# Performance work log

Hardware: AMD Instinct MI355X
Metric: run time of the kernel (lower is better)

The kernel has to match this reference:

```python
import jax, jax.numpy as jnp
import numpy as np

B, T, C, H = 4, 4096, 384, 64

def setup_inputs() -> dict:
    key = jax.random.key(0)
    ks = jax.random.split(key, 7)
    return {
        "x": jax.random.normal(ks[0], (B, T, C), dtype=jnp.float32),
        "Wk": jax.random.normal(ks[1], (H, C), dtype=jnp.float32) * 0.05,
        "bk": jax.random.normal(ks[2], (H,), dtype=jnp.float32) * 0.05,
        "Wq": jax.random.normal(ks[3], (H, C), dtype=jnp.float32) * 0.05,
        "bq": jax.random.normal(ks[4], (H,), dtype=jnp.float32) * 0.05,
        "Wv": jax.random.normal(ks[5], (H, C), dtype=jnp.float32) * 0.05,
        "bv": jax.random.normal(ks[6], (H,), dtype=jnp.float32) * 0.05,
    }

def reference(x, Wk, bk, Wq, bq, Wv, bv):
    # Faithful to the source, including its quirks:
    #   - q = self.value(x)   (query uses the VALUE projection; Wq/bq unused)
    #   - scale = C ** -0.5 with C = embedding dim (384), not head dim
    #   - dropout in eval mode (identity)
    Bb, Tt, Cc = x.shape
    k = x @ Wk.T + bk                                  # (B,T,H)
    q = x @ Wv.T + bv                                  # (B,T,H)  <- bug reproduced
    scale = jnp.float32(Cc) ** -0.5
    scores = jnp.einsum('bth,bsh->bts', q, k) * scale  # (B,T,T)
    mask = jnp.tril(jnp.ones((Tt, Tt), dtype=bool))    # causal mask
    scores = jnp.where(mask, scores, jnp.float32(-jnp.inf))
    w = jax.nn.softmax(scores, axis=-1)                # (B,T,T)
    v = x @ Wv.T + bv                                  # (B,T,H)
    return jnp.einsum('bts,bsh->bth', w, v)            # (B,T,H)
```

## Files before the change

### kernel.cpp

```cpp
#include <hip/hip_runtime.h>

#define T_SEQ 4096
#define CDIM 384

typedef __attribute__((ext_vector_type(8))) short short8;
typedef __attribute__((ext_vector_type(4))) short short4e;
typedef __attribute__((ext_vector_type(4))) float float4e;

#define KSCALE 0.05103103630798288f
#define KE (KSCALE * 1.4426950408889634f)

__device__ inline unsigned short f2bf(float f) {
  unsigned u = __builtin_bit_cast(unsigned, f);
  u += 0x7FFFu + ((u >> 16) & 1u);
  return (unsigned short)(u >> 16);
}

__device__ inline void dma16(const void* g, void* l) {
  __builtin_amdgcn_global_load_lds(
      (const __attribute__((address_space(1))) unsigned int*)g,
      (__attribute__((address_space(3))) unsigned int*)l, 16, 0, 0);
}

__global__ __launch_bounds__(128) void proj_kernel(
    const float* __restrict__ x, const float* __restrict__ Wk, const float* __restrict__ bk,
    const float* __restrict__ Wv, const float* __restrict__ bv,
    unsigned short* __restrict__ Ktil, unsigned short* __restrict__ Qrow,
    unsigned short* __restrict__ Vtil) {
  __shared__ alignas(16) unsigned short Wl[2][128 * 40];
  const int tid = threadIdx.x;
  const int lane = tid & 63;
  const int w = tid >> 6;
  const int lid = lane & 15, quad = lane >> 4;
  const int rowbase = blockIdx.x * 32 + w * 16;
  const float* xr = x + (size_t)(rowbase + lid) * CDIM;

  float4e wreg[8];
  int wcol[8], wpart[8];
#pragma unroll
  for (int i = 0; i < 8; i++) {
    const int f = tid + 128 * i;
    wcol[i] = f >> 3; wpart[i] = f & 7;
  }
  auto wload = [&](int kc) {
#pragma unroll
    for (int i = 0; i < 8; i++) {
      const float* wsrc = (wcol[i] < 64)
          ? (Wk + (size_t)wcol[i] * CDIM + kc * 32 + wpart[i] * 4)
          : (Wv + (size_t)(wcol[i] - 64) * CDIM + kc * 32 + wpart[i] * 4);
      wreg[i] = *(const float4e*)wsrc;
    }
  };
  auto wstage = [&](int bufi) {
#pragma unroll
    for (int i = 0; i < 8; i++) {
      short4e s;
#pragma unroll
      for (int jj = 0; jj < 4; jj++) s[jj] = (short)f2bf(wreg[i][jj]);
      *(short4e*)(&Wl[bufi][wcol[i] * 40 + wpart[i] * 4]) = s;
    }
  };
  float4e xa0[2], xa1[2];
  auto xload = [&](int kc, int slot) {
    xa0[slot] = *(const float4e*)(xr + kc * 32 + quad * 8);
    xa1[slot] = *(const float4e*)(xr + kc * 32 + quad * 8 + 4);
  };

  wload(0); wstage(0);
  wload(1);
  xload(0, 0); xload(1, 1);
  __syncthreads();

  float4e acc[8];
#pragma unroll
  for (int n = 0; n < 8; n++) acc[n] = (float4e){0.f, 0.f, 0.f, 0.f};

  for (int kc = 0; kc < 12; kc++) {
    if (kc < 11) wstage((kc + 1) & 1);
    if (kc < 10) wload(kc + 2);
    const int slot = kc & 1;
    short8 af;
#pragma unroll
    for (int jj = 0; jj < 4; jj++) {
      af[jj] = (short)f2bf(xa0[slot][jj]);
      af[4 + jj] = (short)f2bf(xa1[slot][jj]);
    }
    if (kc < 10) xload(kc + 2, slot);
#pragma unroll
    for (int n = 0; n < 8; n++) {
      short8 bf = *(const short8*)(&Wl[kc & 1][(n * 16 + lid) * 40 + quad * 8]);
      acc[n] = __builtin_amdgcn_mfma_f32_16x16x32_bf16(af, bf, acc[n], 0, 0, 0);
    }
    __syncthreads();
  }

  const int rbase = rowbase + quad * 4;
#pragma unroll
  for (int n = 0; n < 8; n++) {
    const int col = n * 16 + lid;
    const float bias = (n < 4) ? bk[col] : bv[col - 64];
#pragma unroll
    for (int i = 0; i < 4; i++) {
      const int row = rbase + i;
      const float val = acc[n][i] + bias;
      const int b = row >> 12, t = row & 4095;
      const int kt = t >> 5, ko = t & 31;
      const size_t tile = (size_t)(b * 128 + kt) * 2048;
      if (n < 4) {
        Ktil[tile + ko * 64 + (((col >> 3) ^ (ko & 7)) * 8) + (col & 7)] = f2bf(val);
      } else {
        const int hh = col - 64;
        Qrow[(size_t)row * 64 + hh] = f2bf(val * KE);
        Vtil[tile + hh * 32 + (((ko >> 3) ^ ((hh >> 1) & 3)) * 8) + (ko & 7)] = f2bf(val);
      }
    }
  }
}

__global__ __launch_bounds__(64) void attn_kernel(
    const unsigned short* __restrict__ Ktil, const unsigned short* __restrict__ Qrow,
    const unsigned short* __restrict__ Vtil,
    float* __restrict__ Opart, float* __restrict__ MLpart,
    int seg_tiles, int maxseg, int segshift) {
  __shared__ alignas(16) char lds[18944];
  const int j = blockIdx.x;
  const int b = j & 3;
  const int rest = j >> 2;
  const int qt = 127 - (rest >> segshift);
  const int seg = rest & (maxseg - 1);
  if (seg * seg_tiles > qt) return;

  const int lane = threadIdx.x & 63;
  const int lid = lane & 15, quad = lane >> 4;
  const int q0 = qt * 32;
  const int t0 = seg * seg_tiles;
  const int tend0 = t0 + seg_tiles;
  const int t1 = (qt + 1 < tend0) ? (qt + 1) : tend0;

  const unsigned short* Qb = Qrow + (size_t)(b * T_SEQ + q0) * 64;
  const char* Kg = (const char*)(Ktil + (size_t)(b * 128) * 2048);
  const char* Vg = (const char*)(Vtil + (size_t)(b * 128) * 2048);
  unsigned short* PT = (unsigned short*)(lds + 16384);

  short8 Qf[2][2];
#pragma unroll
  for (int qb = 0; qb < 2; qb++)
#pragma unroll
    for (int h = 0; h < 2; h++)
      Qf[qb][h] = *(const short8*)(Qb + (size_t)(qb * 16 + lid) * 64 + h * 32 + quad * 8);

  float4e Ot[2][4];
  float mrow[2], lrow[2];
#pragma unroll
  for (int qb = 0; qb < 2; qb++) {
#pragma unroll
    for (int cc = 0; cc < 4; cc++) Ot[qb][cc] = (float4e){0.f, 0.f, 0.f, 0.f};
    mrow[qb] = -__builtin_inff(); lrow[qb] = 0.f;
  }
  const float4e zero4 = (float4e){0.f, 0.f, 0.f, 0.f};

  auto issue_tile = [&](int kt, int bufi) {
    const char* kg = Kg + (size_t)kt * 4096;
    const char* vg = Vg + (size_t)kt * 4096;
#pragma unroll
    for (int jj = 0; jj < 4; jj++)
      dma16(kg + jj * 1024 + lane * 16, lds + bufi * 4096 + jj * 1024);
#pragma unroll
    for (int jj = 0; jj < 4; jj++)
      dma16(vg + jj * 1024 + lane * 16, lds + 8192 + bufi * 4096 + jj * 1024);
  };

  issue_tile(t0, 0);

  for (int kt = t0; kt < t1; kt++) {
    const int cb = (kt - t0) & 1, nb = cb ^ 1;
    const int ktn = (kt + 1 < t1) ? kt + 1 : kt;
    issue_tile(ktn, nb);
    __asm__ __volatile__("s_waitcnt vmcnt(8)" ::: "memory");

    short8 Kf[2][2];
#pragma unroll
    for (int kb = 0; kb < 2; kb++) {
      const int row = kb * 16 + lid;
#pragma unroll
      for (int h = 0; h < 2; h++) {
        const int gran = (h * 4 + quad) ^ (row & 7);
        Kf[kb][h] = *(const short8*)(lds + cb * 4096 + row * 128 + gran * 16);
      }
    }
    short8 Vf[4];
#pragma unroll
    for (int cc = 0; cc < 4; cc++) {
      const int hh = cc * 16 + lid;
      const int gran = quad ^ ((hh >> 1) & 3);
      Vf[cc] = *(const short8*)(lds + 8192 + cb * 4096 + hh * 64 + gran * 16);
    }

    float4e St[2][2];
#pragma unroll
    for (int qb = 0; qb < 2; qb++)
#pragma unroll
      for (int kb = 0; kb < 2; kb++) {
        float4e s = __builtin_amdgcn_mfma_f32_16x16x32_bf16(Kf[kb][0], Qf[qb][0], zero4, 0, 0, 0);
        St[qb][kb] = __builtin_amdgcn_mfma_f32_16x16x32_bf16(Kf[kb][1], Qf[qb][1], s, 0, 0, 0);
      }

    const int k0 = kt * 32;
#pragma unroll
    for (int qb = 0; qb < 2; qb++) {
      const int qg = q0 + qb * 16 + lid;
      if (k0 + 31 > q0 + qb * 16) {
#pragma unroll
        for (int kb = 0; kb < 2; kb++) {
          const int kbase = k0 + kb * 16 + quad * 4;
#pragma unroll
          for (int i = 0; i < 4; i++)
            if (kbase + i > qg) St[qb][kb][i] = -__builtin_inff();
        }
      }
      float mx = fmaxf(fmaxf(fmaxf(St[qb][0][0], St[qb][0][1]), fmaxf(St[qb][0][2], St[qb][0][3])),
                       fmaxf(fmaxf(St[qb][1][0], St[qb][1][1]), fmaxf(St[qb][1][2], St[qb][1][3])));
      mx = fmaxf(mx, __shfl_xor(mx, 16));
      mx = fmaxf(mx, __shfl_xor(mx, 32));
      const float mn = fmaxf(mrow[qb], mx);
      const float al = __builtin_amdgcn_exp2f(mrow[qb] - mn);
      float p[2][4], ss = 0.f;
#pragma unroll
      for (int kb = 0; kb < 2; kb++)
#pragma unroll
        for (int i = 0; i < 4; i++) {
          p[kb][i] = __builtin_amdgcn_exp2f(St[qb][kb][i] - mn);
          ss += p[kb][i];
        }
      ss += __shfl_xor(ss, 16);
      ss += __shfl_xor(ss, 32);
      lrow[qb] = lrow[qb] * al + ss;
      mrow[qb] = mn;
#pragma unroll
      for (int kb = 0; kb < 2; kb++) {
        unsigned d0 = (unsigned)f2bf(p[kb][0]) | ((unsigned)f2bf(p[kb][1]) << 16);
        unsigned d1 = (unsigned)f2bf(p[kb][2]) | ((unsigned)f2bf(p[kb][3]) << 16);
        uint2 dd = {d0, d1};
        *(uint2*)(&PT[qb * 640 + lid * 40 + kb * 16 + quad * 4]) = dd;
      }
#pragma unroll
      for (int cc = 0; cc < 4; cc++)
#pragma unroll
        for (int i = 0; i < 4; i++) Ot[qb][cc][i] *= al;
    }
    __builtin_amdgcn_wave_barrier();
    __asm__ __volatile__("s_waitcnt lgkmcnt(0)" ::: "memory");
    short8 Pf[2];
#pragma unroll
    for (int qb = 0; qb < 2; qb++)
      Pf[qb] = *(const short8*)(&PT[qb * 640 + lid * 40 + quad * 8]);
#pragma unroll
    for (int qb = 0; qb < 2; qb++)
#pragma unroll
      for (int cc = 0; cc < 4; cc++)
        Ot[qb][cc] = __builtin_amdgcn_mfma_f32_16x16x32_bf16(Vf[cc], Pf[qb], Ot[qb][cc], 0, 0, 0);
    __builtin_amdgcn_wave_barrier();
  }

  const size_t pidx = (size_t)(b * 128 + qt) * maxseg + seg;
  float* Ob = Opart + pidx * 2048;
#pragma unroll
  for (int qb = 0; qb < 2; qb++)
#pragma unroll
    for (int cc = 0; cc < 4; cc++)
      *(float4e*)(Ob + (size_t)(qb * 16 + lid) * 64 + cc * 16 + quad * 4) = Ot[qb][cc];
  float* ml = MLpart + pidx * 64;
  if (quad == 0) {
#pragma unroll
    for (int qb = 0; qb < 2; qb++) {
      ml[qb * 16 + lid]      = mrow[qb];
      ml[32 + qb * 16 + lid] = lrow[qb];
    }
  }
}

__global__ __launch_bounds__(256) void combine_kernel(
    const float* __restrict__ Opart, const float* __restrict__ MLpart,
    float* __restrict__ out, int segtileshift, int maxseg) {
  const int bq = blockIdx.x;
  const int qt = bq & 127;
  const int nseg = (qt >> segtileshift) + 1;
  const int tid = threadIdx.x;
  __shared__ float sW[4][32], sDen[32];
  const float* ml = MLpart + (size_t)bq * maxseg * 64;
  if (tid < 32) {
    float M = ml[tid];
    for (int s = 1; s < nseg; s++) M = fmaxf(M, ml[s * 64 + tid]);
    float den = 0.f;
    for (int s = 0; s < nseg; s++) {
      const float w = __builtin_amdgcn_exp2f(ml[s * 64 + tid] - M);
      sW[s][tid] = w;
      den += w * ml[s * 64 + 32 + tid];
    }
    sDen[tid] = den;
  }
  __syncthreads();
  const float* Ob = Opart + (size_t)bq * maxseg * 2048;
  float* ob = out + (size_t)bq * 2048;
#pragma unroll
  for (int e = tid; e < 2048; e += 256) {
    const int r = e >> 6;
    float acc = 0.f;
    for (int s = 0; s < nseg; s++) acc += sW[s][r] * Ob[s * 2048 + e];
    ob[e] = acc / sDen[r];
  }
}

extern "C" void kernel_launch(void* const* d_in, const int* in_sizes, int n_in,
                              void* d_out, int out_size, void* d_ws, size_t ws_size,
                              hipStream_t stream) {
  const float* x  = (const float*)d_in[0];
  const float* Wk = (const float*)d_in[1];
  const float* bk = (const float*)d_in[2];
  const float* Wv = (const float*)d_in[5];
  const float* bv = (const float*)d_in[6];
  float* out = (float*)d_out;
  char* ws = (char*)d_ws;

  unsigned short* Ktil = (unsigned short*)(ws);
  unsigned short* Qrow = (unsigned short*)(ws + (2u << 20));
  unsigned short* Vtil = (unsigned short*)(ws + (4u << 20));
  float* Opart = (float*)(ws + (6u << 20));

  int maxseg, segshift, sts, seg_tiles;
  if (ws_size >= ((size_t)24 << 20)) { maxseg = 4; segshift = 2; sts = 5; seg_tiles = 32; }
  else                               { maxseg = 1; segshift = 0; sts = 7; seg_tiles = 128; }
  float* MLpart = (float*)(ws + (6u << 20) + (size_t)maxseg * 512 * 2048 * 4);

  hipLaunchKernelGGL(proj_kernel, dim3(512), dim3(128), 0, stream,
                     x, Wk, bk, Wv, bv, Ktil, Qrow, Vtil);
  hipLaunchKernelGGL(attn_kernel, dim3(4 * 128 * maxseg), dim3(64), 0, stream,
                     Ktil, Qrow, Vtil, Opart, MLpart, seg_tiles, maxseg, segshift);
  hipLaunchKernelGGL(combine_kernel, dim3(512), dim3(256), 0, stream,
                     Opart, MLpart, out, sts, maxseg);
}
```

Measured before the change: 151.5 us.

## Share K/V tile staging across four query-tile waves per block

```diff
diff --git a/kernel.cpp b/kernel.cpp
--- a/kernel.cpp
+++ b/kernel.cpp
@@ -117,164 +117,168 @@
   }
 }
 
-__global__ __launch_bounds__(64) void attn_kernel(
+__global__ __launch_bounds__(256) void attn_kernel(
     const unsigned short* __restrict__ Ktil, const unsigned short* __restrict__ Qrow,
     const unsigned short* __restrict__ Vtil,
     float* __restrict__ Opart, float* __restrict__ MLpart,
     int seg_tiles, int maxseg, int segshift) {
-  __shared__ alignas(16) char lds[18944];
+  __shared__ alignas(16) char lds[26624];
   const int j = blockIdx.x;
   const int b = j & 3;
   const int rest = j >> 2;
-  const int qt = 127 - (rest >> segshift);
+  const int qb = 31 - (rest >> segshift);
   const int seg = rest & (maxseg - 1);
-  if (seg * seg_tiles > qt) return;
-
+  const int t0 = seg * seg_tiles;
+  if (t0 > qb * 4 + 3) return;
+
+  const int wv = threadIdx.x >> 6;
   const int lane = threadIdx.x & 63;
   const int lid = lane & 15, quad = lane >> 4;
+  const int qt = qb * 4 + wv;
   const int q0 = qt * 32;
-  const int t0 = seg * seg_tiles;
-  const int tend0 = t0 + seg_tiles;
-  const int t1 = (qt + 1 < tend0) ? (qt + 1) : tend0;
+  const int tend_b = (qb * 4 + 4 < t0 + seg_tiles) ? qb * 4 + 4 : t0 + seg_tiles;
 
   const unsigned short* Qb = Qrow + (size_t)(b * T_SEQ + q0) * 64;
   const char* Kg = (const char*)(Ktil + (size_t)(b * 128) * 2048);
   const char* Vg = (const char*)(Vtil + (size_t)(b * 128) * 2048);
-  unsigned short* PT = (unsigned short*)(lds + 16384);
+  unsigned short* PT = (unsigned short*)(lds + 16384 + wv * 2560);
 
   short8 Qf[2][2];
 #pragma unroll
-  for (int qb = 0; qb < 2; qb++)
+  for (int qq = 0; qq < 2; qq++)
 #pragma unroll
     for (int h = 0; h < 2; h++)
-      Qf[qb][h] = *(const short8*)(Qb + (size_t)(qb * 16 + lid) * 64 + h * 32 + quad * 8);
+      Qf[qq][h] = *(const short8*)(Qb + (size_t)(qq * 16 + lid) * 64 + h * 32 + quad * 8);
 
   float4e Ot[2][4];
   float mrow[2], lrow[2];
 #pragma unroll
-  for (int qb = 0; qb < 2; qb++) {
-#pragma unroll
-    for (int cc = 0; cc < 4; cc++) Ot[qb][cc] = (float4e){0.f, 0.f, 0.f, 0.f};
-    mrow[qb] = -__builtin_inff(); lrow[qb] = 0.f;
+  for (int qq = 0; qq < 2; qq++) {
+#pragma unroll
+    for (int cc = 0; cc < 4; cc++) Ot[qq][cc] = (float4e){0.f, 0.f, 0.f, 0.f};
+    mrow[qq] = -__builtin_inff(); lrow[qq] = 0.f;
   }
   const float4e zero4 = (float4e){0.f, 0.f, 0.f, 0.f};
 
-  auto issue_tile = [&](int kt, int bufi) {
-    const char* kg = Kg + (size_t)kt * 4096;
-    const char* vg = Vg + (size_t)kt * 4096;
-#pragma unroll
-    for (int jj = 0; jj < 4; jj++)
-      dma16(kg + jj * 1024 + lane * 16, lds + bufi * 4096 + jj * 1024);
-#pragma unroll
-    for (int jj = 0; jj < 4; jj++)
-      dma16(vg + jj * 1024 + lane * 16, lds + 8192 + bufi * 4096 + jj * 1024);
+  auto stage = [&](int kt, int bufi) {
+    dma16(Kg + (size_t)kt * 4096 + wv * 1024 + lane * 16,
+          lds + bufi * 4096 + wv * 1024);
+    dma16(Vg + (size_t)kt * 4096 + wv * 1024 + lane * 16,
+          lds + 8192 + bufi * 4096 + wv * 1024);
   };
 
-  issue_tile(t0, 0);
-
-  for (int kt = t0; kt < t1; kt++) {
+  stage(t0, 0);
+  __asm__ __volatile__("s_waitcnt vmcnt(0)" ::: "memory");
+  __syncthreads();
+
+  for (int kt = t0; kt < tend_b; kt++) {
     const int cb = (kt - t0) & 1, nb = cb ^ 1;
-    const int ktn = (kt + 1 < t1) ? kt + 1 : kt;
-    issue_tile(ktn, nb);
-    __asm__ __volatile__("s_waitcnt vmcnt(8)" ::: "memory");
-
-    short8 Kf[2][2];
-#pragma unroll
-    for (int kb = 0; kb < 2; kb++) {
-      const int row = kb * 16 + lid;
-#pragma unroll
-      for (int h = 0; h < 2; h++) {
-        const int gran = (h * 4 + quad) ^ (row & 7);
-        Kf[kb][h] = *(const short8*)(lds + cb * 4096 + row * 128 + gran * 16);
-      }
-    }
-    short8 Vf[4];
-#pragma unroll
-    for (int cc = 0; cc < 4; cc++) {
-      const int hh = cc * 16 + lid;
-      const int gran = quad ^ ((hh >> 1) & 3);
-      Vf[cc] = *(const short8*)(lds + 8192 + cb * 4096 + hh * 64 + gran * 16);
-    }
-
-    float4e St[2][2];
-#pragma unroll
-    for (int qb = 0; qb < 2; qb++)
+    if (kt + 1 < tend_b) stage(kt + 1, nb);
+
+    if (kt <= qt) {
+      short8 Kf[2][2];
 #pragma unroll
       for (int kb = 0; kb < 2; kb++) {
-        float4e s = __builtin_amdgcn_mfma_f32_16x16x32_bf16(Kf[kb][0], Qf[qb][0], zero4, 0, 0, 0);
-        St[qb][kb] = __builtin_amdgcn_mfma_f32_16x16x32_bf16(Kf[kb][1], Qf[qb][1], s, 0, 0, 0);
-      }
-
-    const int k0 = kt * 32;
-#pragma unroll
-    for (int qb = 0; qb < 2; qb++) {
-      const int qg = q0 + qb * 16 + lid;
-      if (k0 + 31 > q0 + qb * 16) {
+        const int row = kb * 16 + lid;
+#pragma unroll
+        for (int h = 0; h < 2; h++) {
+          const int gran = (h * 4 + quad) ^ (row & 7);
+          Kf[kb][h] = *(const short8*)(lds + cb * 4096 + row * 128 + gran * 16);
+        }
+      }
+      short8 Vf[4];
+#pragma unroll
+      for (int cc = 0; cc < 4; cc++) {
+        const int hh = cc * 16 + lid;
+        const int gran = quad ^ ((hh >> 1) & 3);
+        Vf[cc] = *(const short8*)(lds + 8192 + cb * 4096 + hh * 64 + gran * 16);
+      }
+
+      float4e St[2][2];
+#pragma unroll
+      for (int qq = 0; qq < 2; qq++)
 #pragma unroll
         for (int kb = 0; kb < 2; kb++) {
-          const int kbase = k0 + kb * 16 + quad * 4;
-#pragma unroll
-          for (int i = 0; i < 4; i++)
-            if (kbase + i > qg) St[qb][kb][i] = -__builtin_inff();
+          float4e s = __builtin_amdgcn_mfma_f32_16x16x32_bf16(Kf[kb][0], Qf[qq][0], zero4, 0, 0, 0);
+          St[qq][kb] = __builtin_amdgcn_mfma_f32_16x16x32_bf16(Kf[kb][1], Qf[qq][1], s, 0, 0, 0);
         }
-      }
-      float mx = fmaxf(fmaxf(fmaxf(St[qb][0][0], St[qb][0][1]), fmaxf(St[qb][0][2], St[qb][0][3])),
-                       fmaxf(fmaxf(St[qb][1][0], St[qb][1][1]), fmaxf(St[qb][1][2], St[qb][1][3])));
-      mx = fmaxf(mx, __shfl_xor(mx, 16));
-      mx = fmaxf(mx, __shfl_xor(mx, 32));
-      const float mn = fmaxf(mrow[qb], mx);
-      const float al = __builtin_amdgcn_exp2f(mrow[qb] - mn);
-      float p[2][4], ss = 0.f;
-#pragma unroll
-      for (int kb = 0; kb < 2; kb++)
-#pragma unroll
-        for (int i = 0; i < 4; i++) {
-          p[kb][i] = __builtin_amdgcn_exp2f(St[qb][kb][i] - mn);
-          ss += p[kb][i];
+
+      const int k0 = kt * 32;
+#pragma unroll
+      for (int qq = 0; qq < 2; qq++) {
+        const int qg = q0 + qq * 16 + lid;
+        if (k0 + 31 > q0 + qq * 16) {
+#pragma unroll
+          for (int kb = 0; kb < 2; kb++) {
+            const int kbase = k0 + kb * 16 + quad * 4;
+#pragma unroll
+            for (int i = 0; i < 4; i++)
+              if (kbase + i > qg) St[qq][kb][i] = -__builtin_inff();
+          }
         }
-      ss += __shfl_xor(ss, 16);
-      ss += __shfl_xor(ss, 32);
-      lrow[qb] = lrow[qb] * al + ss;
-      mrow[qb] = mn;
-#pragma unroll
-      for (int kb = 0; kb < 2; kb++) {
-        unsigned d0 = (unsigned)f2bf(p[kb][0]) | ((unsigned)f2bf(p[kb][1]) << 16);
-        unsigned d1 = (unsigned)f2bf(p[kb][2]) | ((unsigned)f2bf(p[kb][3]) << 16);
-        uint2 dd = {d0, d1};
-        *(uint2*)(&PT[qb * 640 + lid * 40 + kb * 16 + quad * 4]) = dd;
-      }
+        float mx = fmaxf(fmaxf(fmaxf(St[qq][0][0], St[qq][0][1]), fmaxf(St[qq][0][2], St[qq][0][3])),
+                         fmaxf(fmaxf(St[qq][1][0], St[qq][1][1]), fmaxf(St[qq][1][2], St[qq][1][3])));
+        mx = fmaxf(mx, __shfl_xor(mx, 16));
+        mx = fmaxf(mx, __shfl_xor(mx, 32));
+        const float mn = fmaxf(mrow[qq], mx);
+        const float al = __builtin_amdgcn_exp2f(mrow[qq] - mn);
+        float p[2][4], ss = 0.f;
+#pragma unroll
+        for (int kb = 0; kb < 2; kb++)
+#pragma unroll
+          for (int i = 0; i < 4; i++) {
+            p[kb][i] = __builtin_amdgcn_exp2f(St[qq][kb][i] - mn);
+            ss += p[kb][i];
+          }
+        ss += __shfl_xor(ss, 16);
+        ss += __shfl_xor(ss, 32);
+        lrow[qq] = lrow[qq] * al + ss;
+        mrow[qq] = mn;
+#pragma unroll
+        for (int kb = 0; kb < 2; kb++) {
+          unsigned d0 = (unsigned)f2bf(p[kb][0]) | ((unsigned)f2bf(p[kb][1]) << 16);
+          unsigned d1 = (unsigned)f2bf(p[kb][2]) | ((unsigned)f2bf(p[kb][3]) << 16);
+          uint2 dd = {d0, d1};
+          *(uint2*)(&PT[qq * 640 + lid * 40 + kb * 16 + quad * 4]) = dd;
+        }
+#pragma unroll
+        for (int cc = 0; cc < 4; cc++)
+#pragma unroll
+          for (int i = 0; i < 4; i++) Ot[qq][cc][i] *= al;
+      }
+      __builtin_amdgcn_wave_barrier();
+      __asm__ __volatile__("s_waitcnt lgkmcnt(0)" ::: "memory");
+      short8 Pf[2];
+#pragma unroll
+      for (int qq = 0; qq < 2; qq++)
+        Pf[qq] = *(const short8*)(&PT[qq * 640 + lid * 40 + quad * 8]);
+#pragma unroll
+      for (int qq = 0; qq < 2; qq++)
+#pragma unroll
+        for (int cc = 0; cc < 4; cc++)
+          Ot[qq][cc] = __builtin_amdgcn_mfma_f32_16x16x32_bf16(Vf[cc], Pf[qq], Ot[qq][cc], 0, 0, 0);
+      __builtin_amdgcn_wave_barrier();
+    }
+
+    __asm__ __volatile__("s_waitcnt vmcnt(0)" ::: "memory");
+    __syncthreads();
+  }
+
+  if (qt >= t0) {
+    const size_t pidx = (size_t)(b * 128 + qt) * maxseg + seg;
+    float* Ob = Opart + pidx * 2048;
+#pragma unroll
+    for (int qq = 0; qq < 2; qq++)
 #pragma unroll
       for (int cc = 0; cc < 4; cc++)
-#pragma unroll
-        for (int i = 0; i < 4; i++) Ot[qb][cc][i] *= al;
-    }
-    __builtin_amdgcn_wave_barrier();
-    __asm__ __volatile__("s_waitcnt lgkmcnt(0)" ::: "memory");
-    short8 Pf[2];
-#pragma unroll
-    for (int qb = 0; qb < 2; qb++)
-      Pf[qb] = *(const short8*)(&PT[qb * 640 + lid * 40 + quad * 8]);
-#pragma unroll
-    for (int qb = 0; qb < 2; qb++)
-#pragma unroll
-      for (int cc = 0; cc < 4; cc++)
-        Ot[qb][cc] = __builtin_amdgcn_mfma_f32_16x16x32_bf16(Vf[cc], Pf[qb], Ot[qb][cc], 0, 0, 0);
-    __builtin_amdgcn_wave_barrier();
-  }
-
-  const size_t pidx = (size_t)(b * 128 + qt) * maxseg + seg;
-  float* Ob = Opart + pidx * 2048;
-#pragma unroll
-  for (int qb = 0; qb < 2; qb++)
-#pragma unroll
-    for (int cc = 0; cc < 4; cc++)
-      *(float4e*)(Ob + (size_t)(qb * 16 + lid) * 64 + cc * 16 + quad * 4) = Ot[qb][cc];
-  float* ml = MLpart + pidx * 64;
-  if (quad == 0) {
-#pragma unroll
-    for (int qb = 0; qb < 2; qb++) {
-      ml[qb * 16 + lid]      = mrow[qb];
-      ml[32 + qb * 16 + lid] = lrow[qb];
+        *(float4e*)(Ob + (size_t)(qq * 16 + lid) * 64 + cc * 16 + quad * 4) = Ot[qq][cc];
+    float* ml = MLpart + pidx * 64;
+    if (quad == 0) {
+#pragma unroll
+      for (int qq = 0; qq < 2; qq++) {
+        ml[qq * 16 + lid]      = mrow[qq];
+        ml[32 + qq * 16 + lid] = lrow[qq];
+      }
     }
   }
 }
@@ -286,7 +290,7 @@
   const int qt = bq & 127;
   const int nseg = (qt >> segtileshift) + 1;
   const int tid = threadIdx.x;
-  __shared__ float sW[4][32], sDen[32];
+  __shared__ float sW[8][32], sDen[32];
   const float* ml = MLpart + (size_t)bq * maxseg * 64;
   if (tid < 32) {
     float M = ml[tid];
@@ -328,13 +332,14 @@
   float* Opart = (float*)(ws + (6u << 20));
 
   int maxseg, segshift, sts, seg_tiles;
-  if (ws_size >= ((size_t)24 << 20)) { maxseg = 4; segshift = 2; sts = 5; seg_tiles = 32; }
-  else                               { maxseg = 1; segshift = 0; sts = 7; seg_tiles = 128; }
+  if (ws_size >= ((size_t)40 << 20))      { maxseg = 8; segshift = 3; sts = 4; seg_tiles = 16; }
+  else if (ws_size >= ((size_t)24 << 20)) { maxseg = 4; segshift = 2; sts = 5; seg_tiles = 32; }
+  else                                    { maxseg = 1; segshift = 0; sts = 7; seg_tiles = 128; }
   float* MLpart = (float*)(ws + (6u << 20) + (size_t)maxseg * 512 * 2048 * 4);
 
   hipLaunchKernelGGL(proj_kernel, dim3(512), dim3(128), 0, stream,
                      x, Wk, bk, Wv, bv, Ktil, Qrow, Vtil);
-  hipLaunchKernelGGL(attn_kernel, dim3(4 * 128 * maxseg), dim3(64), 0, stream,
+  hipLaunchKernelGGL(attn_kernel, dim3(4 * 32 * maxseg), dim3(256), 0, stream,
                      Ktil, Qrow, Vtil, Opart, MLpart, seg_tiles, maxseg, segshift);
   hipLaunchKernelGGL(combine_kernel, dim3(512), dim3(256), 0, stream,
                      Opart, MLpart, out, sts, maxseg);
```

Result: slower. 155.6 us (+2.7%).
